# Kernel optimization log

Measured on AMD Instinct MI355X. Metric: run time of the kernel, lower is better.

The kernel has to match this reference:

```python
import jax, jax.numpy as jnp
import numpy as np

D = 64      # node_input_dim == node_hidden_dim
EIN = 16    # edge_input_dim
EH = 64     # edge_hidden_dim
NL, NR = 5000, 15000
EL, ER = 50000, 150000
STEPS = 6
EPS = 1e-5
SLOPE = 0.01


def _ln(x, g, b):
    mu = jnp.mean(x, axis=-1, keepdims=True)
    v = jnp.mean((x - mu) ** 2, axis=-1, keepdims=True)
    return (x - mu) / jnp.sqrt(v + EPS) * g + b


def _lrelu(x):
    return jnp.where(x > 0, x, SLOPE * x)


def setup_inputs() -> dict:
    key = jax.random.key(0)
    ks = jax.random.split(key, 32)

    def n(k, shape, fan_in):
        return jax.random.normal(k, shape, jnp.float32) * (fan_in ** -0.5)

    return {
        'lig_n_feat': jax.random.normal(ks[0], (NL, D), jnp.float32),
        'lig_e_feat': jax.random.normal(ks[1], (EL, EIN), jnp.float32),
        'lig_src': jax.random.randint(ks[2], (EL,), 0, NL),
        'lig_dst': jax.random.randint(ks[3], (EL,), 0, NL),
        'rec_n_feat': jax.random.normal(ks[4], (NR, D), jnp.float32),
        'rec_e_feat': jax.random.normal(ks[5], (ER, EIN), jnp.float32),
        'rec_src': jax.random.randint(ks[6], (ER,), 0, NR),
        'rec_dst': jax.random.randint(ks[7], (ER,), 0, NR),
        'mask': jax.random.uniform(ks[8], (NL, NR), jnp.float32),
        # linear0
        'W0': n(ks[9], (D, D), D), 'b0': jnp.zeros((D,), jnp.float32),
        # edge network: Linear(EIN,EH) -> ReLU -> Linear(EH, D*D)
        'We1': n(ks[10], (EH, EIN), EIN), 'be1': jnp.zeros((EH,), jnp.float32),
        'We2': n(ks[11], (D * D, EH), EH), 'be2': jnp.zeros((D * D,), jnp.float32),
        # NNConv residual fc (no bias) and conv bias
        'resW': n(ks[12], (D, D), D), 'conv_b': jnp.zeros((D,), jnp.float32),
        # message layer Linear(2D, D)
        'msgW': n(ks[13], (D, 2 * D), 2 * D), 'msgb': jnp.zeros((D,), jnp.float32),
        # attention projections (no bias)
        'Qlig': n(ks[14], (D, D), D), 'Klig': n(ks[15], (D, D), D), 'Vlig': n(ks[16], (D, D), D),
        'Qrec': n(ks[17], (D, D), D), 'Krec': n(ks[18], (D, D), D), 'Vrec': n(ks[19], (D, D), D),
        # final LayerNorms
        'g_lig': jnp.ones((D,), jnp.float32), 'b_lig': jnp.zeros((D,), jnp.float32),
        'g_rec': jnp.ones((D,), jnp.float32), 'b_rec': jnp.zeros((D,), jnp.float32),
    }


def _gather_branch(x, efeat, src, dst, n_nodes, W0, b0, We1, be1, We2, be2, resW, conv_b, msgW, msgb):
    # per-edge weight matrices from edge MLP: [E, D, D] (in x out)
    We = jax.nn.relu(efeat @ We1.T + be1) @ We2.T + be2
    We = We.reshape(-1, D, D)
    h = jax.nn.relu(x @ W0.T + b0)
    for _ in range(STEPS):
        msg = jnp.einsum('ei,eio->eo', h[src], We)          # gather + per-edge transform
        agg = jax.ops.segment_sum(msg, dst, num_segments=n_nodes)  # scatter-sum
        m = jax.nn.relu(agg + h @ resW.T + conv_b)           # NNConv residual + bias, relu
        h = jnp.concatenate([m, h], axis=1) @ msgW.T + msgb  # message_layer
    return h + x


def reference(lig_n_feat, lig_e_feat, lig_src, lig_dst, rec_n_feat, rec_e_feat, rec_src, rec_dst,
              mask, W0, b0, We1, be1, We2, be2, resW, conv_b, msgW, msgb,
              Qlig, Klig, Vlig, Qrec, Krec, Vrec, g_lig, b_lig, g_rec, b_rec):
    lig_Fv = _gather_branch(lig_n_feat, lig_e_feat, lig_src, lig_dst, NL,
                            W0, b0, We1, be1, We2, be2, resW, conv_b, msgW, msgb)
    rec_Fv = _gather_branch(rec_n_feat, rec_e_feat, rec_src, rec_dst, NR,
                            W0, b0, We1, be1, We2, be2, resW, conv_b, msgW, msgb)
    hl = _ln(lig_Fv, g_lig, b_lig)
    hr = _ln(rec_Fv, g_rec, b_rec)
    # lig attends to rec
    ql, kr, vr = _lrelu(hl @ Qlig.T), _lrelu(hr @ Krec.T), hr @ Vrec.T
    a = mask * (ql @ kr.T) - 1000.0 * (1.0 - mask)
    att_lig = jax.nn.softmax(a, axis=1) @ vr
    # rec attends to lig
    qr, kl, vl = _lrelu(hr @ Qrec.T), _lrelu(hl @ Klig.T), hl @ Vlig.T
    mt = mask.T
    a2 = mt * (qr @ kl.T) - 1000.0 * (1.0 - mt)
    att_rec = jax.nn.softmax(a2, axis=1) @ vl
    return (_ln(att_lig, g_lig, b_lig), _ln(att_rec, g_rec, b_rec))
```

## Files before the change

kernel.cpp:

```cpp
#include <hip/hip_runtime.h>
#include <hip/hip_bf16.h>

typedef unsigned short ushort_t;
typedef __attribute__((ext_vector_type(8))) short short8_t;
typedef __attribute__((ext_vector_type(4))) float f32x4;
typedef __attribute__((ext_vector_type(4))) unsigned uint4_t;
typedef __attribute__((ext_vector_type(2))) unsigned uint2_t;

#define NLIG 5000
#define NREC 15000
#define NTOT 20000
#define ELIG 50000
#define EREC 150000
#define ETOT 200000
#define VSTRIDE 20160
#define NB0 313
#define NB1 938
#define SEGLEN 2500
#define NSEG0 6
#define NSEG1 2
#define NBA (NB0*NSEG0 + NB1*NSEG1)
#define PSLOT 1056

__device__ __forceinline__ float us2f(ushort_t u){
  union { float f; unsigned int i; } x; x.i = ((unsigned int)u) << 16; return x.f;
}
__device__ __forceinline__ ushort_t f2us(float f){
  __hip_bfloat16 b = __float2bfloat16(f);
  return *reinterpret_cast<ushort_t*>(&b);
}
__device__ __forceinline__ unsigned pkbf(float a, float b){
  return (unsigned)f2us(a) | ((unsigned)f2us(b) << 16);
}
__device__ __forceinline__ float wsum64(float v){
#pragma unroll
  for (int s = 32; s >= 1; s >>= 1) v += __shfl_xor(v, s, 64);
  return v;
}
__device__ __forceinline__ f32x4 mfma32(short8_t a, short8_t b, f32x4 c){
  return __builtin_amdgcn_mfma_f32_16x16x32_bf16(a, b, c, 0, 0, 0);
}
__device__ __forceinline__ int geti(const int* __restrict__ p, int i, int i64){
  return i64 ? p[2*i] : p[i];
}

__global__ void kdetect2(const unsigned* __restrict__ xw, const unsigned* __restrict__ iw,
                         int* __restrict__ flagp){
  const int lane = threadIdx.x;
  unsigned w = xw[lane];
  int e0 = (int)((w >> 7) & 0xFF);
  int hit = (e0 >= 100 && e0 <= 134) ? 1 : 0;
  int zodd = ((lane & 1) && iw[lane] == 0u) ? 1 : 0;
#pragma unroll
  for (int s = 32; s >= 1; s >>= 1){
    hit  += __shfl_xor(hit,  s, 64);
    zodd += __shfl_xor(zodd, s, 64);
  }
  if (lane == 0){
    flagp[0] = (hit  >= 40) ? 1 : 0;
    flagp[1] = (zodd >= 24) ? 1 : 0;
  }
}

__global__ void ksent(float* __restrict__ out, int n, float c){
  int i = blockIdx.x*256 + threadIdx.x;
  if (i < n) out[i] = c;
}

__global__ void kcvt_x(const void* __restrict__ lx, const void* __restrict__ rx,
                       const int* __restrict__ flagp, float* __restrict__ xall){
  const int flag = flagp[0];
  const int idx = blockIdx.x*256 + threadIdx.x;
  const void* src; int local;
  if (idx < NLIG*64){ src = lx; local = idx; } else { src = rx; local = idx - NLIG*64; }
  float v;
  if (flag) v = us2f(((const ushort_t*)src)[local]);
  else      v = ((const float*)src)[local];
  xall[idx] = v;
}

struct Srcs { const void* p[20]; };
__global__ void kcvt_w(Srcs S, const int* __restrict__ flagp, float* __restrict__ wcvt){
  const int bounds[21] = {0,4096,4160,5184,5248,267392,271488,275584,275648,283840,
                          283904,288000,292096,296192,300288,304384,308480,308544,308608,308672,308736};
  const int flag = flagp[0];
  const int idx = blockIdx.x*256 + threadIdx.x;
  if (idx >= 308736) return;
  int seg = 0;
#pragma unroll
  for (int s = 1; s < 20; ++s) if (idx >= bounds[s]) seg = s;
  const void* src = S.p[0];
#pragma unroll
  for (int s = 1; s < 20; ++s) if (seg == s) src = S.p[s];
  const int local = idx - bounds[seg];
  float v;
  if (flag) v = us2f(((const ushort_t*)src)[local]);
  else      v = ((const float*)src)[local];
  wcvt[idx] = v;
}

#define W_W0    0
#define W_B0    4096
#define W_WE1   4160
#define W_BE1   5184
#define W_WE2   5248
#define W_BE2   267392
#define W_RESW  271488
#define W_CONVB 275584
#define W_MSGW  275648
#define W_MSGB  283840
#define W_QLIG  283904
#define W_KLIG  288000
#define W_VLIG  292096
#define W_QREC  296192
#define W_KREC  300288
#define W_VREC  304384
#define W_GLIG  308480
#define W_BLIG  308544
#define W_GREC  308608
#define W_BREC  308672

__global__ void kWpk(const float* __restrict__ We2f, ushort_t* __restrict__ Wpk){
  int oidx = blockIdx.x*256 + threadIdx.x;
  int j = oidx & 7, lane = (oidx >> 3) & 63, p = (oidx >> 9) & 1;
  int t = (oidx >> 10) & 3, kb = oidx >> 12;
  int o = t*16 + (lane & 15);
  int gik = kb*32 + (lane >> 4)*8 + j;
  int i = gik >> 6, k = gik & 63;
  float v = We2f[(size_t)(i*64 + o)*64 + k];
  ushort_t hi = f2us(v);
  Wpk[oidx] = p ? f2us(v - us2f(hi)) : hi;
}

__global__ void kh0(const float* __restrict__ xall, const float* __restrict__ W0f,
                    const float* __restrict__ b0f, float* __restrict__ h){
  __shared__ float xr[4][64];
  const int lane = threadIdx.x & 63, wv = threadIdx.x >> 6;
  const int n = blockIdx.x*4 + wv;
  xr[wv][lane] = xall[(size_t)n*64 + lane];
  __syncthreads();
  float acc = b0f[lane];
  const float* wr = W0f + lane*64;
#pragma unroll
  for (int i = 0; i < 64; ++i) acc += xr[wv][i] * wr[i];
  h[(size_t)n*64 + lane] = acc > 0.f ? acc : 0.f;
}

__global__ void khist(const int* __restrict__ ldst, const int* __restrict__ rdst,
                      const int* __restrict__ flagp, int* __restrict__ counts){
  const int i64 = flagp[1];
  const int e = blockIdx.x*256 + threadIdx.x;
  if (e >= ETOT) return;
  int dstg = (e < ELIG) ? geti(ldst, e, i64) : geti(rdst, e - ELIG, i64) + NLIG;
  atomicAdd(&counts[dstg], 1);
}

__global__ __launch_bounds__(1024) void kscan(const int* __restrict__ counts, int* __restrict__ offs){
  __shared__ int part[1024];
  const int tid = threadIdx.x;
  const int PER = 20;
  int loc[PER]; int s = 0;
#pragma unroll
  for (int j = 0; j < PER; ++j){ int idx = tid*PER + j; int v = (idx < NTOT) ? counts[idx] : 0; loc[j] = s; s += v; }
  part[tid] = s;
  __syncthreads();
  for (int d = 1; d < 1024; d <<= 1){
    int add = (tid >= d) ? part[tid - d] : 0;
    __syncthreads();
    part[tid] += add;
    __syncthreads();
  }
  int pre = (tid > 0) ? part[tid - 1] : 0;
#pragma unroll
  for (int j = 0; j < PER; ++j){ int idx = tid*PER + j; if (idx < NTOT) offs[idx] = pre + loc[j]; }
  if (tid == 1023) offs[NTOT] = part[1023];
}

__global__ void kfill(const int* __restrict__ lsrc, const int* __restrict__ ldst,
                      const int* __restrict__ rsrc, const int* __restrict__ rdst,
                      const void* __restrict__ lef, const void* __restrict__ ref_,
                      const int* __restrict__ offs, int* __restrict__ cursor,
                      const int* __restrict__ flagp,
                      int* __restrict__ e_srcn, float* __restrict__ ef_srt){
  const int flag = flagp[0];
  const int i64  = flagp[1];
  const int e = blockIdx.x*256 + threadIdx.x;
  if (e >= ETOT) return;
  int srcg, dstg, le; const void* efb;
  if (e < ELIG){ srcg = geti(lsrc, e, i64); dstg = geti(ldst, e, i64); efb = lef; le = e; }
  else {
    int e2 = e - ELIG;
    srcg = geti(rsrc, e2, i64) + NLIG; dstg = geti(rdst, e2, i64) + NLIG; efb = ref_; le = e2;
  }
  int pos = offs[dstg] + atomicAdd(&cursor[dstg], 1);
  e_srcn[pos] = srcg;
  float* efd = ef_srt + (size_t)pos*16;
  if (flag){
    const ushort_t* efp = (const ushort_t*)efb + (size_t)le*16;
#pragma unroll
    for (int c = 0; c < 16; ++c) efd[c] = us2f(efp[c]);
  } else {
    const float* efp = (const float*)efb + (size_t)le*16;
#pragma unroll
    for (int c = 0; c < 16; ++c) efd[c] = efp[c];
  }
}

__global__ void kz(const float* __restrict__ ef_srt, const float* __restrict__ We1f,
                   const float* __restrict__ be1f, float* __restrict__ z_srt){
  const int lane = threadIdx.x & 63, wv = threadIdx.x >> 6;
  const int e = blockIdx.x*4 + wv;
  const float* efp = ef_srt + (size_t)e*16;
  float acc = be1f[lane];
  const float* wr = We1f + lane*16;
#pragma unroll
  for (int c = 0; c < 16; ++c) acc += efp[c] * wr[c];
  z_srt[(size_t)e*64 + lane] = acc > 0.f ? acc : 0.f;
}

#define SROW 2080
#define SLO  (16*SROW)
__global__ __launch_bounds__(1024)
void kstep(const float* __restrict__ hin, float* __restrict__ hout,
           const int* __restrict__ offs, const int* __restrict__ e_srcn,
           const float* __restrict__ z_srt,
           const ushort_t* __restrict__ Wpk,
           const float* __restrict__ resWf, const float* __restrict__ convbf,
           const float* __restrict__ msgWf, const float* __restrict__ msgbf,
           const float* __restrict__ be2f){
  __shared__ alignas(16) char sbuf[2*SLO];
  __shared__ float h_lds[1024];
  __shared__ float Hs_lds[1024];
  __shared__ float m_lds[1024];
  __shared__ float cbf[64], mbf[64];

  const int tid = threadIdx.x, lane = tid & 63, wv = tid >> 6;
  const int n0 = blockIdx.x * 16;

  h_lds[tid] = hin[(size_t)n0*64 + tid];
  if (tid < 64){ cbf[tid] = convbf[tid]; mbf[tid] = msgbf[tid]; }

  float sacc[64];
#pragma unroll
  for (int i = 0; i < 64; ++i) sacc[i] = 0.f;
  float hs = 0.f;
  {
    const int v = n0 + wv;
    const int jb = offs[v], je = offs[v+1];
    for (int j = jb; j < je; ++j){
      const int sn = e_srcn[j];
      const float zl = z_srt[(size_t)j*64 + lane];
      hs += hin[(size_t)sn*64 + lane];
      const float4* hp = (const float4*)(hin + (size_t)sn*64);
#pragma unroll
      for (int i4 = 0; i4 < 16; ++i4){
        float4 hv = hp[i4];
        sacc[i4*4+0] += hv.x * zl;
        sacc[i4*4+1] += hv.y * zl;
        sacc[i4*4+2] += hv.z * zl;
        sacc[i4*4+3] += hv.w * zl;
      }
    }
    Hs_lds[wv*64 + lane] = hs;
  }

  const int r15 = lane & 15, g4 = lane >> 4;
  const int tW = wv & 3, kq = wv >> 2;
  f32x4 acc; acc[0]=0.f; acc[1]=0.f; acc[2]=0.f; acc[3]=0.f;
#pragma unroll
  for (int c = 0; c < 4; ++c){
#pragma unroll
    for (int ii = 0; ii < 16; ++ii){
      float v = sacc[c*16 + ii];
      ushort_t hi16 = f2us(v);
      unsigned off = (unsigned)(wv*SROW + (ii*64 + lane)*2);
      *(ushort_t*)(sbuf + off) = hi16;
      *(ushort_t*)(sbuf + SLO + off) = f2us(v - us2f(hi16));
    }
    __syncthreads();
    for (int kk = 0; kk < 8; ++kk){
      const int lk = kq*256 + kk*32;
      const int kb = c*32 + kq*8 + kk;
      const unsigned aoff = (unsigned)(r15*SROW + (lk + g4*8)*2);
      const short8_t ah = *(const short8_t*)(sbuf + aoff);
      const short8_t al = *(const short8_t*)(sbuf + SLO + aoff);
      const ushort_t* bp = Wpk + (size_t)(kb*4 + tW)*1024 + lane*8;
      const short8_t bh = *(const short8_t*)(bp);
      const short8_t bl = *(const short8_t*)(bp + 512);
      acc = mfma32(ah, bh, acc);
      acc = mfma32(ah, bl, acc);
      acc = mfma32(al, bh, acc);
    }
    __syncthreads();
  }

  float* redf  = (float*)sbuf;
  float* be2s  = (float*)(sbuf + 16384);
  float* resWt = (float*)(sbuf + 32768);
#pragma unroll
  for (int q = 0; q < 4; ++q)
    redf[kq*1024 + (g4*4 + q)*64 + tW*16 + r15] = acc[q];
  for (int idx = tid; idx < 4096; idx += 1024){
    be2s[idx] = be2f[idx];
    resWt[(idx & 63)*65 + (idx >> 6)] = resWf[idx];
  }
  __syncthreads();
  {
    float aggv = cbf[lane];
#pragma unroll
    for (int k4 = 0; k4 < 4; ++k4) aggv += redf[k4*1024 + wv*64 + lane];
    float t1 = 0.f, t2 = 0.f;
#pragma unroll 8
    for (int i = 0; i < 64; ++i){
      t1 += Hs_lds[wv*64 + i] * be2s[i*64 + lane];
      t2 += h_lds[wv*64 + i]  * resWt[i*65 + lane];
    }
    float mv = aggv + t1 + t2;
    m_lds[wv*64 + lane] = mv > 0.f ? mv : 0.f;
  }
  __syncthreads();
  float* msgWt = (float*)sbuf;
  for (int idx = tid; idx < 8192; idx += 1024)
    msgWt[(idx & 127)*65 + (idx >> 7)] = msgWf[idx];
  __syncthreads();
  {
    float hn = mbf[lane];
#pragma unroll 8
    for (int i = 0; i < 64; ++i){
      hn += m_lds[wv*64 + i] * msgWt[i*65 + lane];
      hn += h_lds[wv*64 + i] * msgWt[(64 + i)*65 + lane];
    }
    hout[(size_t)(n0 + wv)*64 + lane] = hn;
  }
}

__global__ void kfvproj(const float* __restrict__ h, const float* __restrict__ xall,
    const float* __restrict__ wcvt,
    ushort_t* __restrict__ qbh, ushort_t* __restrict__ qbl,
    ushort_t* __restrict__ kbh, ushort_t* __restrict__ kbl,
    ushort_t* __restrict__ vbT){
  __shared__ float hr[4][64];
  const int lane = threadIdx.x & 63, wv = threadIdx.x >> 6;
  const int n = blockIdx.x*4 + wv;
  const bool isLig = n < NLIG;
  const float fv = h[(size_t)n*64 + lane] + xall[(size_t)n*64 + lane];
  const float mu = wsum64(fv) * (1.f/64.f);
  const float dd = fv - mu;
  const float var = wsum64(dd*dd) * (1.f/64.f);
  const float gg = wcvt[(isLig ? W_GLIG : W_GREC) + lane];
  const float bb = wcvt[(isLig ? W_BLIG : W_BREC) + lane];
  const float hl = dd * rsqrtf(var + 1e-5f) * gg + bb;
  hr[wv][lane] = hl;
  __syncthreads();
  const float* Qw = wcvt + (isLig ? W_QLIG : W_QREC) + lane*64;
  const float* Kw = wcvt + (isLig ? W_KLIG : W_KREC) + lane*64;
  const float* Vw = wcvt + (isLig ? W_VLIG : W_VREC) + lane*64;
  float qa = 0.f, ka = 0.f, va = 0.f;
#pragma unroll
  for (int i = 0; i < 64; ++i){
    const float hv = hr[wv][i];
    qa += hv * Qw[i];
    ka += hv * Kw[i];
    va += hv * Vw[i];
  }
  qa = qa > 0.f ? qa : 0.01f*qa;
  ka = ka > 0.f ? ka : 0.01f*ka;
  const size_t o = (size_t)n*64 + lane;
  ushort_t qh = f2us(qa); qbh[o] = qh; qbl[o] = f2us(qa - us2f(qh));
  ushort_t kh = f2us(ka); kbh[o] = kh; kbl[o] = f2us(ka - us2f(kh));
  vbT[(size_t)lane*VSTRIDE + n] = f2us(va);
}

__global__ __launch_bounds__(512)
void kattn4(const ushort_t* __restrict__ qbh, const ushort_t* __restrict__ qbl,
            const ushort_t* __restrict__ kbh, const ushort_t* __restrict__ kbl,
            const ushort_t* __restrict__ vbT, const void* __restrict__ maskp,
            const int* __restrict__ flagp, float* __restrict__ pbuf){
  __shared__ float slab[8][2][512];

  const int flag = flagp[0];
  const int tid = threadIdx.x, lane = tid & 63, wv = tid >> 6;
  const int gw = blockIdx.x*8 + wv;
  if (gw >= NBA) return;
  const int dirn = (gw < NB0*NSEG0) ? 0 : 1;
  int bid, seg;
  if (dirn == 0){ bid = gw / NSEG0; seg = gw - bid*NSEG0; }
  else { const int ix = gw - NB0*NSEG0; bid = ix / NSEG1; seg = ix - bid*NSEG1; }
  const int R   = dirn ? NREC : NLIG;
  const int C   = dirn ? NLIG : NREC;
  const int RNB = dirn ? NLIG : 0;
  const int CNB = dirn ? 0 : NLIG;
  const int cs  = seg*SEGLEN;
  const int ce  = cs + SEGLEN;

  const int r15 = lane & 15, g4 = lane >> 4;
  const int rbase = bid*16;
  int rn = rbase + r15; if (rn > R-1) rn = R-1;

  const ushort_t* qph = qbh + (size_t)(RNB + rn)*64;
  const ushort_t* qpl = qbl + (size_t)(RNB + rn)*64;
  const short8_t qh0a = *(const short8_t*)(qph + g4*8);
  const short8_t qh0b = *(const short8_t*)(qph + 32 + g4*8);
  const short8_t ql0a = *(const short8_t*)(qpl + g4*8);
  const short8_t ql0b = *(const short8_t*)(qpl + 32 + g4*8);

  const int srcA = (((g4 & 1) * 2)     << 4) + r15;
  const int srcB = (((g4 & 1) * 2 + 1) << 4) + r15;
  const bool hiBank = (g4 >> 1) != 0;

  auto d0_load = [&](int cb, float4 &va, float4 &vb){
    int cA = cb + g4*4;      if (cA > C-4) cA = C-4;
    int cB = cb + 16 + g4*4; if (cB > C-4) cB = C-4;
    if (flag){
      const ushort_t* mrow = (const ushort_t*)maskp + (size_t)rn*NREC;
      const uint2_t wa = *(const uint2_t*)(mrow + cA);
      const uint2_t wb = *(const uint2_t*)(mrow + cB);
      va.x = us2f((ushort_t)(wa[0] & 0xFFFF)); va.y = us2f((ushort_t)(wa[0] >> 16));
      va.z = us2f((ushort_t)(wa[1] & 0xFFFF)); va.w = us2f((ushort_t)(wa[1] >> 16));
      vb.x = us2f((ushort_t)(wb[0] & 0xFFFF)); vb.y = us2f((ushort_t)(wb[0] >> 16));
      vb.z = us2f((ushort_t)(wb[1] & 0xFFFF)); vb.w = us2f((ushort_t)(wb[1] >> 16));
    } else {
      const float* mrow = (const float*)maskp + (size_t)rn*NREC;
      va = *(const float4*)(mrow + cA);
      vb = *(const float4*)(mrow + cB);
    }
  };
  const int s_c = lane >> 1, s_h = lane & 1;
  auto d1_load = [&](int cb, float4 &va, float4 &vb){
    int c = cb + s_c; if (c > C-1) c = C-1;
    int r0 = rbase + s_h*8; if (r0 > R-8) r0 = R-8;
    const size_t base = (size_t)c*NREC + r0;
    if (flag){
      const ushort_t* mp = (const ushort_t*)maskp + base;
      const short8_t v8 = *(const short8_t*)mp;
      va.x = us2f((ushort_t)v8[0]); va.y = us2f((ushort_t)v8[1]);
      va.z = us2f((ushort_t)v8[2]); va.w = us2f((ushort_t)v8[3]);
      vb.x = us2f((ushort_t)v8[4]); vb.y = us2f((ushort_t)v8[5]);
      vb.z = us2f((ushort_t)v8[6]); vb.w = us2f((ushort_t)v8[7]);
    } else {
      const float* mp = (const float*)maskp + base;
      va = *(const float4*)mp;
      vb = *(const float4*)(mp + 4);
    }
  };
  auto d1_write = [&](int b, const float4 &va, const float4 &vb){
    float* s = &slab[wv][b][s_c*16 + s_h*8];
    *(float4*)s = va; *(float4*)(s + 4) = vb;
  };

  float mrun = -1e30f, lrun = 0.f;
  f32x4 oacc[4];
#pragma unroll
  for (int t = 0; t < 4; ++t){ oacc[t][0]=0.f; oacc[t][1]=0.f; oacc[t][2]=0.f; oacc[t][3]=0.f; }

  float4 pA, pB;
  if (dirn == 0) d0_load(cs, pA, pB);
  else { d1_load(cs, pA, pB); d1_write(0, pA, pB); d1_load(cs + 32, pA, pB); }

  int buf = 0;
  for (int cb = cs; cb < ce; cb += 32){
    float mv0[4], mv1[4];
    if (dirn == 0){
      mv0[0]=pA.x; mv0[1]=pA.y; mv0[2]=pA.z; mv0[3]=pA.w;
      mv1[0]=pB.x; mv1[1]=pB.y; mv1[2]=pB.z; mv1[3]=pB.w;
      if (cb + 32 < ce) d0_load(cb + 32, pA, pB);
    } else {
      const float* s = &slab[wv][buf][0];
#pragma unroll
      for (int j = 0; j < 4; ++j){
        mv0[j] = s[(g4*4 + j)*16 + r15];
        mv1[j] = s[(16 + g4*4 + j)*16 + r15];
      }
      if (cb + 32 < ce){
        d1_write(buf ^ 1, pA, pB);
        if (cb + 64 < ce) d1_load(cb + 64, pA, pB);
      }
      buf ^= 1;
    }

    int cn0 = cb + r15;      if (cn0 > C-1) cn0 = C-1;
    int cn1 = cb + 16 + r15; if (cn1 > C-1) cn1 = C-1;
    const ushort_t* kp0h = kbh + (size_t)(CNB + cn0)*64;
    const ushort_t* kp0l = kbl + (size_t)(CNB + cn0)*64;
    const ushort_t* kp1h = kbh + (size_t)(CNB + cn1)*64;
    const ushort_t* kp1l = kbl + (size_t)(CNB + cn1)*64;
    f32x4 st0; st0[0]=0.f; st0[1]=0.f; st0[2]=0.f; st0[3]=0.f;
    f32x4 st1 = st0;
    {
      short8_t ka_ = *(const short8_t*)(kp0h + g4*8);
      short8_t kb_ = *(const short8_t*)(kp0h + 32 + g4*8);
      st0 = mfma32(ka_, qh0a, st0); st0 = mfma32(kb_, qh0b, st0);
      st0 = mfma32(ka_, ql0a, st0); st0 = mfma32(kb_, ql0b, st0);
      short8_t kc_ = *(const short8_t*)(kp0l + g4*8);
      short8_t kd_ = *(const short8_t*)(kp0l + 32 + g4*8);
      st0 = mfma32(kc_, qh0a, st0); st0 = mfma32(kd_, qh0b, st0);
    }
    {
      short8_t ka_ = *(const short8_t*)(kp1h + g4*8);
      short8_t kb_ = *(const short8_t*)(kp1h + 32 + g4*8);
      st1 = mfma32(ka_, qh0a, st1); st1 = mfma32(kb_, qh0b, st1);
      st1 = mfma32(ka_, ql0a, st1); st1 = mfma32(kb_, ql0b, st1);
      short8_t kc_ = *(const short8_t*)(kp1l + g4*8);
      short8_t kd_ = *(const short8_t*)(kp1l + 32 + g4*8);
      st1 = mfma32(kc_, qh0a, st1); st1 = mfma32(kd_, qh0b, st1);
    }
    float sv0[4], sv1[4]; float tmax = -1e30f;
#pragma unroll
    for (int j = 0; j < 4; ++j){
      const int c0 = cb + g4*4 + j, c1 = cb + 16 + g4*4 + j;
      sv0[j] = (c0 < ce) ? mv0[j] * (st0[j] + 1000.f) : -1e30f;
      sv1[j] = (c1 < ce) ? mv1[j] * (st1[j] + 1000.f) : -1e30f;
      tmax = fmaxf(tmax, fmaxf(sv0[j], sv1[j]));
    }
    tmax = fmaxf(tmax, __shfl_xor(tmax, 16, 64));
    tmax = fmaxf(tmax, __shfl_xor(tmax, 32, 64));
    const float mnew = fmaxf(mrun, tmax);
    const float corr = __expf(mrun - mnew);
    float ps0[4], ps1[4], psum = 0.f;
#pragma unroll
    for (int j = 0; j < 4; ++j){
      ps0[j] = __expf(sv0[j] - mnew); psum += ps0[j];
      ps1[j] = __expf(sv1[j] - mnew); psum += ps1[j];
    }
    psum += __shfl_xor(psum, 16, 64);
    psum += __shfl_xor(psum, 32, 64);
    lrun = lrun * corr + psum;
    mrun = mnew;
    const unsigned pk0 = pkbf(ps0[0], ps0[1]);
    const unsigned pk1 = pkbf(ps0[2], ps0[3]);
    const unsigned pk2 = pkbf(ps1[0], ps1[1]);
    const unsigned pk3 = pkbf(ps1[2], ps1[3]);
    const unsigned a0 = (unsigned)__shfl((int)pk0, srcA, 64);
    const unsigned a2 = (unsigned)__shfl((int)pk2, srcA, 64);
    const unsigned a1 = (unsigned)__shfl((int)pk1, srcA, 64);
    const unsigned a3 = (unsigned)__shfl((int)pk3, srcA, 64);
    const unsigned b0 = (unsigned)__shfl((int)pk0, srcB, 64);
    const unsigned b2 = (unsigned)__shfl((int)pk2, srcB, 64);
    const unsigned b1 = (unsigned)__shfl((int)pk1, srcB, 64);
    const unsigned b3 = (unsigned)__shfl((int)pk3, srcB, 64);
    uint4_t pw;
    pw[0] = hiBank ? a2 : a0;
    pw[1] = hiBank ? a3 : a1;
    pw[2] = hiBank ? b2 : b0;
    pw[3] = hiBank ? b3 : b1;
    const short8_t pf8 = *reinterpret_cast<const short8_t*>(&pw);
    const ushort_t* vtb = vbT + (size_t)(CNB + cb + g4*8);
#pragma unroll
    for (int t = 0; t < 4; ++t){
#pragma unroll
      for (int q = 0; q < 4; ++q) oacc[t][q] *= corr;
      const short8_t af = *(const short8_t*)(vtb + (size_t)(t*16 + r15)*VSTRIDE);
      oacc[t] = mfma32(af, pf8, oacc[t]);
    }
  }

  float* ps = pbuf + (size_t)gw * PSLOT;
  if (g4 == 0){ ps[r15] = mrun; ps[16 + r15] = lrun; }
#pragma unroll
  for (int t = 0; t < 4; ++t)
#pragma unroll
    for (int q = 0; q < 4; ++q)
      ps[32 + r15*64 + t*16 + g4*4 + q] = oacc[t][q];
}

__global__ __launch_bounds__(64)
void kcomb(const float* __restrict__ pbuf, const float* __restrict__ wcvt,
           float* __restrict__ out){
  const int rb = blockIdx.x;
  const int lane = threadIdx.x;
  const int dirn = (rb < NB0) ? 0 : 1;
  const int bid  = dirn ? (rb - NB0) : rb;
  const int R    = dirn ? NREC : NLIG;
  const int nseg = dirn ? NSEG1 : NSEG0;
  const int slot0= dirn ? (NB0*NSEG0 + bid*NSEG1) : (bid*NSEG0);
  const float* gwf = wcvt + (dirn ? W_GREC : W_GLIG);
  const float* bwf = wcvt + (dirn ? W_BREC : W_BLIG);
  float* outp = out + (size_t)(dirn ? NLIG : 0)*64;
  const int rbase = bid * 16;

  for (int rr = 0; rr < 16; ++rr){
    const int rg = rbase + rr;
    if (rg >= R) break;
    float mstar = -1e30f;
    for (int s = 0; s < nseg; ++s)
      mstar = fmaxf(mstar, pbuf[(size_t)(slot0 + s)*PSLOT + rr]);
    float lstar = 0.f, ov = 0.f;
    for (int s = 0; s < nseg; ++s){
      const float* psl = pbuf + (size_t)(slot0 + s)*PSLOT;
      const float e = __expf(psl[rr] - mstar);
      lstar += psl[16 + rr] * e;
      ov    += psl[32 + rr*64 + lane] * e;
    }
    const float att = ov / lstar;
    const float mu = wsum64(att) * (1.f/64.f);
    const float dd = att - mu;
    const float var = wsum64(dd*dd) * (1.f/64.f);
    const float y = dd * rsqrtf(var + 1e-5f) * gwf[lane] + bwf[lane];
    outp[(size_t)rg*64 + lane] = y;
  }
}

extern "C" void kernel_launch(void* const* d_in, const int* in_sizes, int n_in,
                              void* d_out, int out_size, void* d_ws, size_t ws_size,
                              hipStream_t stream){
  const int expsz[29] = {320000,800000,50000,50000,960000,2400000,150000,150000,75000000,
                         4096,64,1024,64,262144,4096,4096,64,8192,64,
                         4096,4096,4096,4096,4096,4096,64,64,64,64};
  bool ok = (n_in == 29);
  if (ok) for (int i = 0; i < 29; ++i) if (in_sizes[i] != expsz[i]) ok = false;
  if (!ok){
    ksent<<<(out_size + 255)/256, 256, 0, stream>>>((float*)d_out, out_size, 10.0f);
    return;
  }

  const void* lig_n = d_in[0];
  const void* lig_e = d_in[1];
  const int* lig_src = (const int*)d_in[2];
  const int* lig_dst = (const int*)d_in[3];
  const void* rec_n = d_in[4];
  const void* rec_e = d_in[5];
  const int* rec_src = (const int*)d_in[6];
  const int* rec_dst = (const int*)d_in[7];
  const void* mask = d_in[8];

  char* p = (char*)d_ws;
  auto carve = [&](size_t bytes)->char*{ char* r = p; p += (bytes + 255) & ~(size_t)255; return r; };
  float*    xall  = (float*)   carve((size_t)NTOT*64*4);
  float*    wcvt  = (float*)   carve((size_t)308736*4);
  float*    h_a   = (float*)   carve((size_t)NTOT*64*4);
  float*    h_b   = (float*)   carve((size_t)NTOT*64*4);
  ushort_t* Wpk   = (ushort_t*)carve((size_t)524288*2);
  ushort_t* qbh   = (ushort_t*)carve((size_t)NTOT*64*2);
  ushort_t* qbl   = (ushort_t*)carve((size_t)NTOT*64*2);
  ushort_t* kbh   = (ushort_t*)carve((size_t)NTOT*64*2);
  ushort_t* kbl   = (ushort_t*)carve((size_t)NTOT*64*2);
  ushort_t* vbT   = (ushort_t*)carve((size_t)64*VSTRIDE*2);
  int*      flag  = (int*)     carve(256);
  int*      counts= (int*)     carve((size_t)2*NTOT*4);
  int*      cursor= counts + NTOT;
  int*      offs  = (int*)     carve((size_t)(NTOT+1)*4);
  int*      e_srcn= (int*)     carve((size_t)ETOT*4);
  float*    ef_srt= (float*)   carve((size_t)ETOT*16*4);
  float*    z_srt = (float*)   carve((size_t)ETOT*64*4);
  float*    pbuf  = (float*)   carve((size_t)NBA*PSLOT*4);

  if ((size_t)(p - (char*)d_ws) > ws_size){
    ksent<<<(out_size + 255)/256, 256, 0, stream>>>((float*)d_out, out_size, 20.0f);
    return;
  }

  Srcs S;
  for (int i = 0; i < 20; ++i) S.p[i] = d_in[9 + i];

  hipMemsetAsync(counts, 0, (size_t)2*NTOT*4, stream);
  hipMemsetAsync(vbT, 0, (size_t)64*VSTRIDE*2, stream);
  kdetect2<<<1, 64, 0, stream>>>((const unsigned*)lig_n, (const unsigned*)lig_src, flag);
  kcvt_x<<<NTOT*64/256, 256, 0, stream>>>(lig_n, rec_n, flag, xall);
  kcvt_w<<<(308736 + 255)/256, 256, 0, stream>>>(S, flag, wcvt);
  kWpk<<<2048, 256, 0, stream>>>(wcvt + W_WE2, Wpk);
  kh0<<<NTOT/4, 256, 0, stream>>>(xall, wcvt + W_W0, wcvt + W_B0, h_a);
  khist<<<(ETOT + 255)/256, 256, 0, stream>>>(lig_dst, rec_dst, flag, counts);
  kscan<<<1, 1024, 0, stream>>>(counts, offs);
  kfill<<<(ETOT + 255)/256, 256, 0, stream>>>(lig_src, lig_dst, rec_src, rec_dst,
                                              lig_e, rec_e, offs, cursor, flag, e_srcn, ef_srt);
  kz<<<ETOT/4, 256, 0, stream>>>(ef_srt, wcvt + W_WE1, wcvt + W_BE1, z_srt);
  float* hi = h_a; float* ho = h_b;
  for (int s = 0; s < 6; ++s){
    kstep<<<NTOT/16, 1024, 0, stream>>>(hi, ho, offs, e_srcn, z_srt, Wpk,
                                        wcvt + W_RESW, wcvt + W_CONVB,
                                        wcvt + W_MSGW, wcvt + W_MSGB, wcvt + W_BE2);
    float* t = hi; hi = ho; ho = t;
  }
  kfvproj<<<NTOT/4, 256, 0, stream>>>(hi, xall, wcvt, qbh, qbl, kbh, kbl, vbT);
  kattn4<<<(NBA + 7)/8, 512, 0, stream>>>(qbh, qbl, kbh, kbl, vbT, mask, flag, pbuf);
  kcomb<<<NB0 + NB1, 64, 0, stream>>>(pbuf, wcvt, (float*)d_out);
}
```

Before: 2.221 ms.

## Halve attention column segments, add split-pass gather kernel, alias partial buffer

```diff
diff --git a/kernel.cpp b/kernel.cpp
--- a/kernel.cpp
+++ b/kernel.cpp
@@ -16,9 +16,9 @@
 #define VSTRIDE 20160
 #define NB0 313
 #define NB1 938
-#define SEGLEN 2500
-#define NSEG0 6
-#define NSEG1 2
+#define SEGLEN 5000
+#define NSEG0 3
+#define NSEG1 1
 #define NBA (NB0*NSEG0 + NB1*NSEG1)
 #define PSLOT 1056
 
@@ -220,6 +220,84 @@
 
 #define SROW 2080
 #define SLO  (16*SROW)
+
+__device__ __forceinline__
+void kstep_tail(char* sbuf, float* h_lds, float* Hs_lds, float* m_lds,
+                float* cbf, float* mbf, float (&sacc)[64],
+                int tid, int lane, int wv, int n0,
+                const ushort_t* __restrict__ Wpk,
+                const float* __restrict__ resWf, const float* __restrict__ msgWf,
+                const float* __restrict__ be2f, float* __restrict__ hout){
+  const int r15 = lane & 15, g4 = lane >> 4;
+  const int tW = wv & 3, kq = wv >> 2;
+  f32x4 acc; acc[0]=0.f; acc[1]=0.f; acc[2]=0.f; acc[3]=0.f;
+#pragma unroll
+  for (int c = 0; c < 4; ++c){
+#pragma unroll
+    for (int ii = 0; ii < 16; ++ii){
+      float v = sacc[c*16 + ii];
+      ushort_t hi16 = f2us(v);
+      unsigned off = (unsigned)(wv*SROW + (ii*64 + lane)*2);
+      *(ushort_t*)(sbuf + off) = hi16;
+      *(ushort_t*)(sbuf + SLO + off) = f2us(v - us2f(hi16));
+    }
+    __syncthreads();
+    for (int kk = 0; kk < 8; ++kk){
+      const int lk = kq*256 + kk*32;
+      const int kb = c*32 + kq*8 + kk;
+      const unsigned aoff = (unsigned)(r15*SROW + (lk + g4*8)*2);
+      const short8_t ah = *(const short8_t*)(sbuf + aoff);
+      const short8_t al = *(const short8_t*)(sbuf + SLO + aoff);
+      const ushort_t* bp = Wpk + (size_t)(kb*4 + tW)*1024 + lane*8;
+      const short8_t bh = *(const short8_t*)(bp);
+      const short8_t bl = *(const short8_t*)(bp + 512);
+      acc = mfma32(ah, bh, acc);
+      acc = mfma32(ah, bl, acc);
+      acc = mfma32(al, bh, acc);
+    }
+    __syncthreads();
+  }
+
+  float* redf  = (float*)sbuf;
+  float* be2s  = (float*)(sbuf + 16384);
+  float* resWt = (float*)(sbuf + 32768);
+#pragma unroll
+  for (int q = 0; q < 4; ++q)
+    redf[kq*1024 + (g4*4 + q)*64 + tW*16 + r15] = acc[q];
+  for (int idx = tid; idx < 4096; idx += 1024){
+    be2s[idx] = be2f[idx];
+    resWt[(idx & 63)*65 + (idx >> 6)] = resWf[idx];
+  }
+  __syncthreads();
+  {
+    float aggv = cbf[lane];
+#pragma unroll
+    for (int k4 = 0; k4 < 4; ++k4) aggv += redf[k4*1024 + wv*64 + lane];
+    float t1 = 0.f, t2 = 0.f;
+#pragma unroll 8
+    for (int i = 0; i < 64; ++i){
+      t1 += Hs_lds[wv*64 + i] * be2s[i*64 + lane];
+      t2 += h_lds[wv*64 + i]  * resWt[i*65 + lane];
+    }
+    float mv = aggv + t1 + t2;
+    m_lds[wv*64 + lane] = mv > 0.f ? mv : 0.f;
+  }
+  __syncthreads();
+  float* msgWt = (float*)sbuf;
+  for (int idx = tid; idx < 8192; idx += 1024)
+    msgWt[(idx & 127)*65 + (idx >> 7)] = msgWf[idx];
+  __syncthreads();
+  {
+    float hn = mbf[lane];
+#pragma unroll 8
+    for (int i = 0; i < 64; ++i){
+      hn += m_lds[wv*64 + i] * msgWt[i*65 + lane];
+      hn += h_lds[wv*64 + i] * msgWt[(64 + i)*65 + lane];
+    }
+    hout[(size_t)(n0 + wv)*64 + lane] = hn;
+  }
+}
+
 __global__ __launch_bounds__(1024)
 void kstep(const float* __restrict__ hin, float* __restrict__ hout,
            const int* __restrict__ offs, const int* __restrict__ e_srcn,
@@ -263,75 +341,68 @@
     }
     Hs_lds[wv*64 + lane] = hs;
   }
-
-  const int r15 = lane & 15, g4 = lane >> 4;
-  const int tW = wv & 3, kq = wv >> 2;
-  f32x4 acc; acc[0]=0.f; acc[1]=0.f; acc[2]=0.f; acc[3]=0.f;
-#pragma unroll
-  for (int c = 0; c < 4; ++c){
-#pragma unroll
-    for (int ii = 0; ii < 16; ++ii){
-      float v = sacc[c*16 + ii];
-      ushort_t hi16 = f2us(v);
-      unsigned off = (unsigned)(wv*SROW + (ii*64 + lane)*2);
-      *(ushort_t*)(sbuf + off) = hi16;
-      *(ushort_t*)(sbuf + SLO + off) = f2us(v - us2f(hi16));
-    }
-    __syncthreads();
-    for (int kk = 0; kk < 8; ++kk){
-      const int lk = kq*256 + kk*32;
-      const int kb = c*32 + kq*8 + kk;
-      const unsigned aoff = (unsigned)(r15*SROW + (lk + g4*8)*2);
-      const short8_t ah = *(const short8_t*)(sbuf + aoff);
-      const short8_t al = *(const short8_t*)(sbuf + SLO + aoff);
-      const ushort_t* bp = Wpk + (size_t)(kb*4 + tW)*1024 + lane*8;
-      const short8_t bh = *(const short8_t*)(bp);
-      const short8_t bl = *(const short8_t*)(bp + 512);
-      acc = mfma32(ah, bh, acc);
-      acc = mfma32(ah, bl, acc);
-      acc = mfma32(al, bh, acc);
-    }
-    __syncthreads();
-  }
-
-  float* redf  = (float*)sbuf;
-  float* be2s  = (float*)(sbuf + 16384);
-  float* resWt = (float*)(sbuf + 32768);
-#pragma unroll
-  for (int q = 0; q < 4; ++q)
-    redf[kq*1024 + (g4*4 + q)*64 + tW*16 + r15] = acc[q];
-  for (int idx = tid; idx < 4096; idx += 1024){
-    be2s[idx] = be2f[idx];
-    resWt[(idx & 63)*65 + (idx >> 6)] = resWf[idx];
-  }
-  __syncthreads();
+  kstep_tail(sbuf, h_lds, Hs_lds, m_lds, cbf, mbf, sacc, tid, lane, wv, n0,
+             Wpk, resWf, msgWf, be2f, hout);
+}
+
+__global__ __launch_bounds__(1024)
+void kstep2(const float* __restrict__ hin, float* __restrict__ hout,
+            const int* __restrict__ offs, const int* __restrict__ e_srcn,
+            const float* __restrict__ z_srt,
+            const ushort_t* __restrict__ Wpk,
+            const float* __restrict__ resWf, const float* __restrict__ convbf,
+            const float* __restrict__ msgWf, const float* __restrict__ msgbf,
+            const float* __restrict__ be2f){
+  __shared__ alignas(16) char sbuf[2*SLO];
+  __shared__ float h_lds[1024];
+  __shared__ float Hs_lds[1024];
+  __shared__ float m_lds[1024];
+  __shared__ float cbf[64], mbf[64];
+
+  const int tid = threadIdx.x, lane = tid & 63, wv = tid >> 6;
+  const int n0 = blockIdx.x * 16;
+
+  h_lds[tid] = hin[(size_t)n0*64 + tid];
+  if (tid < 64){ cbf[tid] = convbf[tid]; mbf[tid] = msgbf[tid]; }
+
+  float sacc[64];
+#pragma unroll
+  for (int i = 0; i < 64; ++i) sacc[i] = 0.f;
+  float hs = 0.f;
   {
-    float aggv = cbf[lane];
-#pragma unroll
-    for (int k4 = 0; k4 < 4; ++k4) aggv += redf[k4*1024 + wv*64 + lane];
-    float t1 = 0.f, t2 = 0.f;
-#pragma unroll 8
-    for (int i = 0; i < 64; ++i){
-      t1 += Hs_lds[wv*64 + i] * be2s[i*64 + lane];
-      t2 += h_lds[wv*64 + i]  * resWt[i*65 + lane];
-    }
-    float mv = aggv + t1 + t2;
-    m_lds[wv*64 + lane] = mv > 0.f ? mv : 0.f;
-  }
-  __syncthreads();
-  float* msgWt = (float*)sbuf;
-  for (int idx = tid; idx < 8192; idx += 1024)
-    msgWt[(idx & 127)*65 + (idx >> 7)] = msgWf[idx];
-  __syncthreads();
-  {
-    float hn = mbf[lane];
-#pragma unroll 8
-    for (int i = 0; i < 64; ++i){
-      hn += m_lds[wv*64 + i] * msgWt[i*65 + lane];
-      hn += h_lds[wv*64 + i] * msgWt[(64 + i)*65 + lane];
-    }
-    hout[(size_t)(n0 + wv)*64 + lane] = hn;
-  }
+    const int v = n0 + wv;
+    const int jb = offs[v], je = offs[v+1];
+    for (int j = jb; j < je; ++j){
+      const int sn = e_srcn[j];
+      const float zl = z_srt[(size_t)j*64 + lane];
+      hs += hin[(size_t)sn*64 + lane];
+      const float4* hp = (const float4*)(hin + (size_t)sn*64);
+#pragma unroll
+      for (int i4 = 0; i4 < 8; ++i4){
+        float4 hv = hp[i4];
+        sacc[i4*4+0] += hv.x * zl;
+        sacc[i4*4+1] += hv.y * zl;
+        sacc[i4*4+2] += hv.z * zl;
+        sacc[i4*4+3] += hv.w * zl;
+      }
+    }
+    for (int j = jb; j < je; ++j){
+      const int sn = e_srcn[j];
+      const float zl = z_srt[(size_t)j*64 + lane];
+      const float4* hp = (const float4*)(hin + (size_t)sn*64 + 32);
+#pragma unroll
+      for (int i4 = 0; i4 < 8; ++i4){
+        float4 hv = hp[i4];
+        sacc[32+i4*4+0] += hv.x * zl;
+        sacc[32+i4*4+1] += hv.y * zl;
+        sacc[32+i4*4+2] += hv.z * zl;
+        sacc[32+i4*4+3] += hv.w * zl;
+      }
+    }
+    Hs_lds[wv*64 + lane] = hs;
+  }
+  kstep_tail(sbuf, h_lds, Hs_lds, m_lds, cbf, mbf, sacc, tid, lane, wv, n0,
+             Wpk, resWf, msgWf, be2f, hout);
 }
 
 __global__ void kfvproj(const float* __restrict__ h, const float* __restrict__ xall,
@@ -385,7 +456,7 @@
   const int dirn = (gw < NB0*NSEG0) ? 0 : 1;
   int bid, seg;
   if (dirn == 0){ bid = gw / NSEG0; seg = gw - bid*NSEG0; }
-  else { const int ix = gw - NB0*NSEG0; bid = ix / NSEG1; seg = ix - bid*NSEG1; }
+  else { bid = gw - NB0*NSEG0; seg = 0; }
   const int R   = dirn ? NREC : NLIG;
   const int C   = dirn ? NLIG : NREC;
   const int RNB = dirn ? NLIG : 0;
@@ -642,7 +713,7 @@
   int*      e_srcn= (int*)     carve((size_t)ETOT*4);
   float*    ef_srt= (float*)   carve((size_t)ETOT*16*4);
   float*    z_srt = (float*)   carve((size_t)ETOT*64*4);
-  float*    pbuf  = (float*)   carve((size_t)NBA*PSLOT*4);
+  float*    pbuf  = ef_srt;
 
   if ((size_t)(p - (char*)d_ws) > ws_size){
     ksent<<<(out_size + 255)/256, 256, 0, stream>>>((float*)d_out, out_size, 20.0f);
@@ -666,9 +737,14 @@
   kz<<<ETOT/4, 256, 0, stream>>>(ef_srt, wcvt + W_WE1, wcvt + W_BE1, z_srt);
   float* hi = h_a; float* ho = h_b;
   for (int s = 0; s < 6; ++s){
-    kstep<<<NTOT/16, 1024, 0, stream>>>(hi, ho, offs, e_srcn, z_srt, Wpk,
-                                        wcvt + W_RESW, wcvt + W_CONVB,
-                                        wcvt + W_MSGW, wcvt + W_MSGB, wcvt + W_BE2);
+    if (s < 3)
+      kstep<<<NTOT/16, 1024, 0, stream>>>(hi, ho, offs, e_srcn, z_srt, Wpk,
+                                          wcvt + W_RESW, wcvt + W_CONVB,
+                                          wcvt + W_MSGW, wcvt + W_MSGB, wcvt + W_BE2);
+    else
+      kstep2<<<NTOT/16, 1024, 0, stream>>>(hi, ho, offs, e_srcn, z_srt, Wpk,
+                                           wcvt + W_RESW, wcvt + W_CONVB,
+                                           wcvt + W_MSGW, wcvt + W_MSGB, wcvt + W_BE2);
     float* t = hi; hi = ho; ho = t;
   }
   kfvproj<<<NTOT/4, 256, 0, stream>>>(hi, xall, wcvt, qbh, qbl, kbh, kbl, vbT);
```

Result: faster. 2.155 ms (-3.0%).
